# Kernel tuning notes

Hardware: AMD Instinct MI355X
Metric: run time of the kernel (lower is better)

## Reference

```python
import jax, jax.numpy as jnp
import numpy as np

POOL = (2, 2)  # pool_size from init


def setup_inputs() -> dict:
    key = jax.random.key(0)
    k1, k2 = jax.random.split(key)
    B, H, W, C = 8, 128, 128, 256
    Ho, Wo = H * POOL[0], W * POOL[1]
    inputs = jax.random.normal(k1, (B, H, W, C), dtype=jnp.float32)
    # argmax-style indices: per-batch offsets into flattened (Ho, Wo, C)
    indices = jax.random.randint(k2, (B, H, W, C), 0, Ho * Wo * C, dtype=jnp.int32)
    return {"inputs": inputs, "indices": indices}


def reference(inputs, indices):
    # Faithful to MaxUnpooling2D.call: scatter pooled values into a
    # zero-initialized tensor of shape (B, H*ph, W*pw, C) at argmax positions.
    B, H, W, C = inputs.shape
    Ho, Wo = H * POOL[0], W * POOL[1]
    flat_out = Ho * Wo * C  # per-batch flat output size
    # add per-batch offset (mirrors batch_range * flat_output_shape[1])
    batch_off = (jnp.arange(B, dtype=indices.dtype) * flat_out)[:, None]
    flat_idx = indices.reshape(B, -1) + batch_off  # [B, H*W*C]
    out = jnp.zeros((B * flat_out,), dtype=inputs.dtype)
    # tf.scatter_nd sums duplicate indices -> .at[].add matches
    out = out.at[flat_idx.reshape(-1)].add(inputs.reshape(-1))
    return out.reshape(B, Ho, Wo, C)
```

## Files before the change

### kernel.cpp

```cpp
#include <hip/hip_runtime.h>
#include <stdint.h>


#define LOG2_REGION 15
#define REGION      (1 << LOG2_REGION)
#define NB          (1 << (24 - LOG2_REGION))
#define NBUCKETS    (8 * NB)
#define SUB         16384
#define BLOCK1      1024
#define GRID1       ((1 << 25) / SUB)
#define PADM        3
#define STAGE_CAP   (SUB + PADM * NB)
#define BLOCK2      1024

__global__ __launch_bounds__(BLOCK1) void bin_pairs(
    const int*   __restrict__ idx,
    const float* __restrict__ val,
    int*         __restrict__ counters,
    uint64_t*    __restrict__ pairs,
    int cap)
{
    __shared__ uint64_t stage[STAGE_CAP];
    __shared__ int hist[NB];
    __shared__ int pos[NB];
    __shared__ int gseg[NB];
    __shared__ int s_total;

    const int tid = threadIdx.x;
    const long long start = (long long)blockIdx.x * SUB;
    const int batch = (int)(start >> 22);
    const int4*   idx4 = (const int4*)(idx + start);
    const float4* val4 = (const float4*)(val + start);

    for (int i = tid; i < NB; i += BLOCK1) hist[i] = 0;
    __syncthreads();

    int4 iv[4];
    #pragma unroll
    for (int it = 0; it < 4; ++it) {
        iv[it] = idx4[it * BLOCK1 + tid];
        atomicAdd(&hist[iv[it].x >> LOG2_REGION], 1);
        atomicAdd(&hist[iv[it].y >> LOG2_REGION], 1);
        atomicAdd(&hist[iv[it].z >> LOG2_REGION], 1);
        atomicAdd(&hist[iv[it].w >> LOG2_REGION], 1);
    }
    __syncthreads();

    if (tid < NB) pos[tid] = (hist[tid] + PADM) & ~PADM;
    __syncthreads();
    for (int off = 1; off < NB; off <<= 1) {
        int v = 0;
        if (tid < NB && tid >= off) v = pos[tid - off];
        __syncthreads();
        if (tid < NB && tid >= off) pos[tid] += v;
        __syncthreads();
    }
    if (tid == NB - 1) s_total = pos[tid];
    int excl = 0, hp = 0;
    if (tid < NB) { hp = (hist[tid] + PADM) & ~PADM; excl = pos[tid] - hp; }
    __syncthreads();
    if (tid < NB) {
        pos[tid] = excl;
        int* gc = counters + batch * NB;
        gseg[tid] = hp ? atomicAdd(&gc[tid], hp) : 0;
    }
    __syncthreads();

    #pragma unroll
    for (int it = 0; it < 4; ++it) {
        float4 vv = val4[it * BLOCK1 + tid];
        int   ia[4] = {iv[it].x, iv[it].y, iv[it].z, iv[it].w};
        float fa[4] = {vv.x, vv.y, vv.z, vv.w};
        #pragma unroll
        for (int k = 0; k < 4; ++k) {
            int b = ia[k] >> LOG2_REGION;
            int l = atomicAdd(&pos[b], 1);
            stage[l] = (uint64_t)(uint32_t)ia[k]
                     | ((uint64_t)__float_as_uint(fa[k]) << 32);
        }
    }
    __syncthreads();

    for (int b = tid; b < NB; b += BLOCK1) {
        int h = hist[b];
        int hp2 = (h + PADM) & ~PADM;
        int st = pos[b];
        for (int j = 0; j < hp2 - h; ++j)
            stage[st + j] = (uint64_t)(uint32_t)(b << LOG2_REGION);
    }
    __syncthreads();

    const int total = s_total;
    uint64_t* pb = pairs + (uint64_t)batch * NB * (uint64_t)cap;
    for (int i = tid; i < total; i += BLOCK1) {
        uint64_t p = stage[i];
        int b = (int)((uint32_t)p >> LOG2_REGION);
        int lstart_b = pos[b] - hist[b];
        int dst = gseg[b] + (i - lstart_b);
        if (dst < cap)
            pb[(uint64_t)b * cap + dst] = p;
    }
}

__global__ __launch_bounds__(BLOCK2) void accumulate(
    const uint64_t* __restrict__ pairs,
    const int*      __restrict__ counters,
    float*          __restrict__ out,
    int cap)
{
    __shared__ float acc[REGION];
    const int b = blockIdx.x;
    const int tid = threadIdx.x;

    float4* acc4 = (float4*)acc;
    for (int i = tid; i < REGION / 4; i += BLOCK2)
        acc4[i] = make_float4(0.f, 0.f, 0.f, 0.f);
    __syncthreads();

    int n = counters[b];
    if (n > cap) n = cap;
    const uint64_t* p = pairs + (uint64_t)b * cap;
    for (int i = tid; i < n; i += BLOCK2) {
        uint64_t v = p[i];
        atomicAdd(&acc[(int)(v & (REGION - 1))],
                  __uint_as_float((uint32_t)(v >> 32)));
    }
    __syncthreads();

    float4* o4 = (float4*)(out + ((long long)b << LOG2_REGION));
    for (int i = tid; i < REGION / 4; i += BLOCK2)
        o4[i] = acc4[i];
}

extern "C" void kernel_launch(void* const* d_in, const int* in_sizes, int n_in,
                              void* d_out, int out_size, void* d_ws, size_t ws_size,
                              hipStream_t stream) {
    const float* in  = (const float*)d_in[0];
    const int*   idx = (const int*)d_in[1];
    float*       out = (float*)d_out;

    int*      counters = (int*)d_ws;
    uint64_t* pairs    = (uint64_t*)((char*)d_ws + 65536);

    int cap = (int)(((ws_size - 65536) / 8) / NBUCKETS);
    if (cap > 16384) cap = 16384;
    cap &= ~PADM;

    hipMemsetAsync(counters, 0, NBUCKETS * sizeof(int), stream);
    bin_pairs<<<GRID1, BLOCK1, 0, stream>>>(idx, in, counters, pairs, cap);
    accumulate<<<NBUCKETS, BLOCK2, 0, stream>>>(pairs, counters, out, cap);
}
```

Before: 922.4 us.

## Halve region size, use wave-shuffle scan, write padding directly to global

```diff
diff --git a/kernel.cpp b/kernel.cpp
--- a/kernel.cpp
+++ b/kernel.cpp
@@ -2,7 +2,7 @@
 #include <stdint.h>
 
 
-#define LOG2_REGION 15
+#define LOG2_REGION 14
 #define REGION      (1 << LOG2_REGION)
 #define NB          (1 << (24 - LOG2_REGION))
 #define NBUCKETS    (8 * NB)
@@ -10,8 +10,7 @@
 #define BLOCK1      1024
 #define GRID1       ((1 << 25) / SUB)
 #define PADM        3
-#define STAGE_CAP   (SUB + PADM * NB)
-#define BLOCK2      1024
+#define BLOCK2      512
 
 __global__ __launch_bounds__(BLOCK1) void bin_pairs(
     const int*   __restrict__ idx,
@@ -20,19 +19,21 @@
     uint64_t*    __restrict__ pairs,
     int cap)
 {
-    __shared__ uint64_t stage[STAGE_CAP];
+    __shared__ uint64_t stage[SUB];
     __shared__ int hist[NB];
     __shared__ int pos[NB];
-    __shared__ int gseg[NB];
-    __shared__ int s_total;
+    __shared__ int delta[NB];
+    __shared__ int wsumI[16];
 
-    const int tid = threadIdx.x;
+    const int tid  = threadIdx.x;
+    const int lane = tid & 63;
+    const int wave = tid >> 6;
     const long long start = (long long)blockIdx.x * SUB;
     const int batch = (int)(start >> 22);
     const int4*   idx4 = (const int4*)(idx + start);
     const float4* val4 = (const float4*)(val + start);
 
-    for (int i = tid; i < NB; i += BLOCK1) hist[i] = 0;
+    hist[tid] = 0;
     __syncthreads();
 
     int4 iv[4];
@@ -46,23 +47,40 @@
     }
     __syncthreads();
 
-    if (tid < NB) pos[tid] = (hist[tid] + PADM) & ~PADM;
+    const int h  = hist[tid];
+    const int hp = (h + PADM) & ~PADM;
+    int v = h;
+    #pragma unroll
+    for (int d = 1; d < 64; d <<= 1) {
+        int u = __shfl_up(v, d);
+        if (lane >= d) v += u;
+    }
+    if (lane == 63) wsumI[wave] = v;
     __syncthreads();
-    for (int off = 1; off < NB; off <<= 1) {
-        int v = 0;
-        if (tid < NB && tid >= off) v = pos[tid - off];
-        __syncthreads();
-        if (tid < NB && tid >= off) pos[tid] += v;
-        __syncthreads();
+    if (tid < 16) {
+        int t = wsumI[tid];
+        #pragma unroll
+        for (int d = 1; d < 16; d <<= 1) {
+            int u = __shfl_up(t, d);
+            if (tid >= d) t += u;
+        }
+        wsumI[tid] = t;
     }
-    if (tid == NB - 1) s_total = pos[tid];
-    int excl = 0, hp = 0;
-    if (tid < NB) { hp = (hist[tid] + PADM) & ~PADM; excl = pos[tid] - hp; }
     __syncthreads();
-    if (tid < NB) {
-        pos[tid] = excl;
-        int* gc = counters + batch * NB;
-        gseg[tid] = hp ? atomicAdd(&gc[tid], hp) : 0;
+    const int lstart = v + (wave ? wsumI[wave - 1] : 0) - h;
+    pos[tid] = lstart;
+    int gbase = 0;
+    if (hp) gbase = atomicAdd(&counters[batch * NB + tid], hp);
+    delta[tid] = gbase - lstart;
+
+    uint64_t* pb = pairs + (uint64_t)batch * NB * (uint64_t)cap;
+
+    {
+        const uint64_t padp = (uint64_t)(uint32_t)(tid << LOG2_REGION);
+        for (int j = h; j < hp; ++j) {
+            int dst = gbase + j;
+            if (dst < cap) pb[(uint64_t)tid * cap + dst] = padp;
+        }
     }
     __syncthreads();
 
@@ -81,22 +99,10 @@
     }
     __syncthreads();
 
-    for (int b = tid; b < NB; b += BLOCK1) {
-        int h = hist[b];
-        int hp2 = (h + PADM) & ~PADM;
-        int st = pos[b];
-        for (int j = 0; j < hp2 - h; ++j)
-            stage[st + j] = (uint64_t)(uint32_t)(b << LOG2_REGION);
-    }
-    __syncthreads();
-
-    const int total = s_total;
-    uint64_t* pb = pairs + (uint64_t)batch * NB * (uint64_t)cap;
-    for (int i = tid; i < total; i += BLOCK1) {
+    for (int i = tid; i < SUB; i += BLOCK1) {
         uint64_t p = stage[i];
         int b = (int)((uint32_t)p >> LOG2_REGION);
-        int lstart_b = pos[b] - hist[b];
-        int dst = gseg[b] + (i - lstart_b);
+        int dst = i + delta[b];
         if (dst < cap)
             pb[(uint64_t)b * cap + dst] = p;
     }
@@ -113,21 +119,25 @@
     const int tid = threadIdx.x;
 
     float4* acc4 = (float4*)acc;
+    #pragma unroll
     for (int i = tid; i < REGION / 4; i += BLOCK2)
         acc4[i] = make_float4(0.f, 0.f, 0.f, 0.f);
     __syncthreads();
 
     int n = counters[b];
     if (n > cap) n = cap;
-    const uint64_t* p = pairs + (uint64_t)b * cap;
-    for (int i = tid; i < n; i += BLOCK2) {
-        uint64_t v = p[i];
-        atomicAdd(&acc[(int)(v & (REGION - 1))],
-                  __uint_as_float((uint32_t)(v >> 32)));
+    const ulonglong2* p2 = (const ulonglong2*)(pairs + (uint64_t)b * cap);
+    for (int i = tid; i < (n >> 1); i += BLOCK2) {
+        ulonglong2 v = p2[i];
+        atomicAdd(&acc[(int)(v.x & (REGION - 1))],
+                  __uint_as_float((uint32_t)(v.x >> 32)));
+        atomicAdd(&acc[(int)(v.y & (REGION - 1))],
+                  __uint_as_float((uint32_t)(v.y >> 32)));
     }
     __syncthreads();
 
     float4* o4 = (float4*)(out + ((long long)b << LOG2_REGION));
+    #pragma unroll
     for (int i = tid; i < REGION / 4; i += BLOCK2)
         o4[i] = acc4[i];
 }
@@ -143,7 +153,7 @@
     uint64_t* pairs    = (uint64_t*)((char*)d_ws + 65536);
 
     int cap = (int)(((ws_size - 65536) / 8) / NBUCKETS);
-    if (cap > 16384) cap = 16384;
+    if (cap > 8192) cap = 8192;
     cap &= ~PADM;
 
     hipMemsetAsync(counters, 0, NBUCKETS * sizeof(int), stream);
```

Result: slower. 958.6 us (+3.9%).
